# Performance work log

Measured on AMD Instinct MI355X. Metric: run time of the kernel, lower is better.

The kernel has to match this reference:

```python
import jax, jax.numpy as jnp
import numpy as np

B, T, F, H = 256, 512, 64, 128


def _uniform(key, shape, stdv):
    return jax.random.uniform(key, shape, jnp.float32, -stdv, stdv)


def setup_inputs() -> dict:
    key = jax.random.key(0)
    ks = jax.random.split(key, 24)
    values = jax.random.normal(ks[0], (B, T, F), jnp.float32)
    masks = (jax.random.uniform(ks[1], (B, T, F)) < 0.8).astype(jnp.float32)
    deltas = jax.random.uniform(ks[2], (B, T, F), jnp.float32)
    labels = (jax.random.uniform(ks[3], (B, 1)) < 0.5).astype(jnp.float32)
    is_train = (jax.random.uniform(ks[4], (B, 1)) < 0.8).astype(jnp.float32)
    sH = 1.0 / np.sqrt(H)
    sF = 1.0 / np.sqrt(F)
    # temp_decay_h: Linear F -> H (stdv = 1/sqrt(out) per reset_parameters)
    W_dh = _uniform(ks[5], (H, F), sH); b_dh = _uniform(ks[6], (H,), sH)
    # temp_decay_x: diag F -> F
    W_dx = _uniform(ks[7], (F, F), sF); b_dx = _uniform(ks[8], (F,), sF)
    # hist_reg: Linear H -> F (torch Linear stdv = 1/sqrt(in))
    W_hr = _uniform(ks[9], (F, H), sH); b_hr = _uniform(ks[10], (F,), sH)
    # feat_reg: F -> F with zeroed diagonal mask
    W_fr = _uniform(ks[11], (F, F), sF); b_fr = _uniform(ks[12], (F,), sF)
    # weight_combine: Linear 2F -> F
    s2F = 1.0 / np.sqrt(2 * F)
    W_wc = _uniform(ks[13], (F, 2 * F), s2F); b_wc = _uniform(ks[14], (F,), s2F)
    # LSTMCell(2F, H): torch init uniform(-1/sqrt(H), 1/sqrt(H)), gate order i,f,g,o
    W_ih = _uniform(ks[15], (4 * H, 2 * F), sH); b_ih = _uniform(ks[16], (4 * H,), sH)
    W_hh = _uniform(ks[17], (4 * H, H), sH); b_hh = _uniform(ks[18], (4 * H,), sH)
    # out: Linear H -> 1
    W_out = _uniform(ks[19], (1, H), sH); b_out = _uniform(ks[20], (1,), sH)
    return dict(values=values, masks=masks, deltas=deltas, labels=labels, is_train=is_train,
                W_dh=W_dh, b_dh=b_dh, W_dx=W_dx, b_dx=b_dx, W_hr=W_hr, b_hr=b_hr,
                W_fr=W_fr, b_fr=b_fr, W_wc=W_wc, b_wc=b_wc,
                W_ih=W_ih, b_ih=b_ih, W_hh=W_hh, b_hh=b_hh, W_out=W_out, b_out=b_out)


def _forward(values, masks, deltas, labels, is_train,
             W_dh, b_dh, W_dx, b_dx, W_hr, b_hr, W_fr, b_fr, W_wc, b_wc,
             W_ih, b_ih, W_hh, b_hh, W_out, b_out):
    eps = 1e-5
    w_dx_diag = jnp.diagonal(W_dx)            # diag mask: W * I
    W_fr_m = W_fr * (1.0 - jnp.eye(F, dtype=W_fr.dtype))  # zero diagonal

    def step(carry, xs):
        h, c, x_loss = carry
        x, m, d = xs                           # each [B, F]
        gamma_h = jnp.exp(-jax.nn.relu(d @ W_dh.T + b_dh))   # [B, H]
        gamma_x = jnp.exp(-jax.nn.relu(d * w_dx_diag + b_dx))  # [B, F]
        h = h * gamma_h
        x_h = h @ W_hr.T + b_hr                # [B, F]
        msum = jnp.sum(m) + eps
        x_loss = x_loss + jnp.sum(jnp.abs(x - x_h) * m) / msum
        x_c = m * x + (1.0 - m) * x_h
        z_h = x_c @ W_fr_m.T + b_fr
        x_loss = x_loss + jnp.sum(jnp.abs(x - z_h) * m) / msum
        alpha = jnp.concatenate([gamma_x, m], axis=1) @ W_wc.T + b_wc
        c_h = alpha * z_h + (1.0 - alpha) * x_h
        x_loss = x_loss + jnp.sum(jnp.abs(x - c_h) * m) / msum
        c_c = m * x + (1.0 - m) * c_h
        inp = jnp.concatenate([c_c, m], axis=1)   # [B, 2F]
        gates = inp @ W_ih.T + b_ih + h @ W_hh.T + b_hh  # [B, 4H]
        i, f, g, o = jnp.split(gates, 4, axis=1)
        c = jax.nn.sigmoid(f) * c + jax.nn.sigmoid(i) * jnp.tanh(g)
        h = jax.nn.sigmoid(o) * jnp.tanh(c)
        return (h, c, x_loss), c_c

    h0 = jnp.zeros((values.shape[0], H), values.dtype)
    c0 = jnp.zeros((values.shape[0], H), values.dtype)
    xs = (jnp.swapaxes(values, 0, 1), jnp.swapaxes(masks, 0, 1), jnp.swapaxes(deltas, 0, 1))
    (h, c, x_loss), imps = jax.lax.scan(step, (h0, c0, jnp.float32(0.0)), xs)
    imputations = jnp.swapaxes(imps, 0, 1)     # [B, T, F]
    y_h = h @ W_out.T + b_out                  # [B, 1] logits
    # stable BCE with logits (matches torch reference formula)
    max_val = jnp.maximum(-y_h, 0.0)
    y_l = y_h - y_h * labels + max_val + jnp.log(jnp.exp(-max_val) + jnp.exp(-y_h - max_val))
    y_loss = jnp.sum(y_l * is_train) / (jnp.sum(is_train) + eps)
    loss = x_loss / T + y_loss * 0.3
    predictions = jax.nn.sigmoid(y_h)
    return loss, predictions, imputations


def reference(values, masks, deltas, labels, is_train,
              W_dh, b_dh, W_dx, b_dx, W_hr, b_hr, W_fr, b_fr, W_wc, b_wc,
              W_ih, b_ih, W_hh, b_hh, W_out, b_out):
    return _forward(values, masks, deltas, labels, is_train,
                    W_dh, b_dh, W_dx, b_dx, W_hr, b_hr, W_fr, b_fr, W_wc, b_wc,
                    W_ih, b_ih, W_hh, b_hh, W_out, b_out)
```

## Files before the change

### kernel.cpp

```cpp
#include <hip/hip_runtime.h>
#include <hip/hip_fp16.h>


#define NBATCH 256
#define NT 512
#define NF 64
#define NH 128

#define WHH_OFF   0u
#define WIH_OFF   131072u
#define WHR_OFF   262144u
#define WFR_OFF   278528u
#define INVMS_OFF 286720u
#define ISTR_OFF  288768u
#define GH_OFF    294912u
#define AL_OFF    33849344u

typedef _Float16 half2_t __attribute__((ext_vector_type(2)));

__device__ __forceinline__ unsigned pack2(float a, float b) {
    __half2 h = __floats2half2_rn(a, b);
    return __builtin_bit_cast(unsigned, h);
}

__device__ __forceinline__ float dot2f(unsigned w, unsigned a, float acc) {
#if __has_builtin(__builtin_amdgcn_fdot2)
    return __builtin_amdgcn_fdot2(__builtin_bit_cast(half2_t, w),
                                  __builtin_bit_cast(half2_t, a), acc, false);
#else
    float2 wf = __half22float2(__builtin_bit_cast(__half2, w));
    float2 af = __half22float2(__builtin_bit_cast(__half2, a));
    return acc + wf.x * af.x + wf.y * af.y;
#endif
}

__device__ __forceinline__ float sigm(float x) { return 1.f / (1.f + __expf(-x)); }
__device__ __forceinline__ float tanh_fast(float x) { return 1.f - 2.f / (__expf(2.f * x) + 1.f); }

__global__ __launch_bounds__(256) void prep_w(const float* __restrict__ Whh,
                                              const float* __restrict__ Wih,
                                              const float* __restrict__ Whr,
                                              const float* __restrict__ Wfr,
                                              unsigned* __restrict__ wsu) {
    int o = blockIdx.x * 256 + threadIdx.x;
    float v0, v1;
    if (o < 32768) {
        int c = o & 3, r = (o >> 2) & 511, cb = o >> 11;
        int col = 8 * cb + 2 * c;
        v0 = Whh[r * 128 + col]; v1 = Whh[r * 128 + col + 1];
    } else if (o < 65536) {
        int o2 = o - 32768;
        int c = o2 & 3, r = (o2 >> 2) & 511, cb = o2 >> 11;
        int col = 8 * cb + 2 * c;
        v0 = Wih[r * 128 + col]; v1 = Wih[r * 128 + col + 1];
    } else if (o < 69632) {
        int o3 = o - 65536;
        int c = o3 & 3, f = (o3 >> 2) & 63, cb = o3 >> 8;
        int col = 8 * cb + 2 * c;
        v0 = Whr[f * 128 + col]; v1 = Whr[f * 128 + col + 1];
    } else if (o < 71680) {
        int o4 = o - 69632;
        int c = o4 & 3, f = (o4 >> 2) & 63, cb = o4 >> 8;
        int col = 8 * cb + 2 * c;
        v0 = (col == f) ? 0.f : Wfr[f * 64 + col];
        v1 = (col + 1 == f) ? 0.f : Wfr[f * 64 + col + 1];
    } else {
        return;
    }
    wsu[o] = pack2(v0, v1);
}

__global__ __launch_bounds__(256) void prep_msum(const float* __restrict__ masks,
                                                 const float* __restrict__ is_train,
                                                 float* __restrict__ invms,
                                                 float* __restrict__ inv_istr,
                                                 float* __restrict__ d_out0) {
    __shared__ float red[256];
    int tid = threadIdx.x;
    int t = blockIdx.x;
    if (t < NT) {
        int f = tid & 63, br = tid >> 6;
        float s = 0.f;
        for (int i = 0; i < 64; i++) {
            int b = br + i * 4;
            s += masks[((size_t)b * NT + t) * NF + f];
        }
        red[tid] = s;
        __syncthreads();
        for (int off = 128; off > 0; off >>= 1) {
            if (tid < off) red[tid] += red[tid + off];
            __syncthreads();
        }
        if (tid == 0) invms[t] = 1.f / (red[0] + 1e-5f);
    } else {
        red[tid] = is_train[tid];
        __syncthreads();
        for (int off = 128; off > 0; off >>= 1) {
            if (tid < off) red[tid] += red[tid + off];
            __syncthreads();
        }
        if (tid == 0) {
            *inv_istr = 1.f / (red[0] + 1e-5f);
            *d_out0 = 0.f;
        }
    }
}

__global__ __launch_bounds__(256) void ga_kernel(const float* __restrict__ deltas,
                                                 const float* __restrict__ masks,
                                                 const float* __restrict__ Wdh,
                                                 const float* __restrict__ bdh,
                                                 const float* __restrict__ Wdx,
                                                 const float* __restrict__ bdx,
                                                 const float* __restrict__ Wwc,
                                                 const float* __restrict__ bwc,
                                                 __half* __restrict__ gh_all,
                                                 __half* __restrict__ al_all) {
    __shared__ unsigned wdhpk[32 * 128];
    __shared__ unsigned wwcpk[64 * 64];
    __shared__ float sbdh[128], sbdx[64], swdx[64], sbwc[64];
    __shared__ float dbuf[64];
    __shared__ __align__(16) unsigned dpk[32], gxpk[32], mpk2[32];
    int tid = threadIdx.x;

    for (int o = tid; o < 4096; o += 256) {
        int j = o & 127, k2 = o >> 7;
        wdhpk[o] = pack2(Wdh[j * 64 + 2 * k2], Wdh[j * 64 + 2 * k2 + 1]);
    }
    for (int o = tid; o < 4096; o += 256) {
        int f = o & 63, k2 = o >> 6;
        wwcpk[o] = pack2(Wwc[f * 128 + 2 * k2], Wwc[f * 128 + 2 * k2 + 1]);
    }
    if (tid < 128) sbdh[tid] = bdh[tid];
    if (tid < 64) {
        sbdx[tid] = bdx[tid];
        swdx[tid] = Wdx[tid * 65];
        sbwc[tid] = bwc[tid];
    }
    __syncthreads();

    for (int i = 0; i < 32; i++) {
        int p = blockIdx.x * 32 + i;
        if (tid < 32) {
            float2 dv = ((const float2*)(deltas + (size_t)p * NF))[tid];
            dbuf[2 * tid] = dv.x; dbuf[2 * tid + 1] = dv.y;
            dpk[tid] = pack2(dv.x, dv.y);
        } else if (tid < 64) {
            int q = tid - 32;
            float2 mv = ((const float2*)(masks + (size_t)p * NF))[q];
            mpk2[q] = pack2(mv.x, mv.y);
        }
        __syncthreads();
        if (tid < 64) {
            float gx = __expf(-fmaxf(dbuf[tid] * swdx[tid] + sbdx[tid], 0.f));
            float oth = __shfl_xor(gx, 1);
            if (!(tid & 1)) gxpk[tid >> 1] = pack2(gx, oth);
        }
        __syncthreads();
        if (tid < 128) {
            float a0 = sbdh[tid], a1 = 0.f;
            #pragma unroll
            for (int k8 = 0; k8 < 8; k8++) {
                uint4 dp = *(const uint4*)&dpk[4 * k8];
                a0 = dot2f(wdhpk[(4 * k8 + 0) * 128 + tid], dp.x, a0);
                a1 = dot2f(wdhpk[(4 * k8 + 1) * 128 + tid], dp.y, a1);
                a0 = dot2f(wdhpk[(4 * k8 + 2) * 128 + tid], dp.z, a0);
                a1 = dot2f(wdhpk[(4 * k8 + 3) * 128 + tid], dp.w, a1);
            }
            gh_all[(size_t)p * NH + tid] = __float2half(__expf(-fmaxf(a0 + a1, 0.f)));
        } else if (tid < 192) {
            int f = tid - 128;
            float a0 = sbwc[f], a1 = 0.f;
            #pragma unroll
            for (int k8 = 0; k8 < 8; k8++) {
                uint4 gp = *(const uint4*)&gxpk[4 * k8];
                a0 = dot2f(wwcpk[(4 * k8 + 0) * 64 + f], gp.x, a0);
                a1 = dot2f(wwcpk[(4 * k8 + 1) * 64 + f], gp.y, a1);
                a0 = dot2f(wwcpk[(4 * k8 + 2) * 64 + f], gp.z, a0);
                a1 = dot2f(wwcpk[(4 * k8 + 3) * 64 + f], gp.w, a1);
            }
            #pragma unroll
            for (int k8 = 0; k8 < 8; k8++) {
                uint4 mp = *(const uint4*)&mpk2[4 * k8];
                a0 = dot2f(wwcpk[(32 + 4 * k8 + 0) * 64 + f], mp.x, a0);
                a1 = dot2f(wwcpk[(32 + 4 * k8 + 1) * 64 + f], mp.y, a1);
                a0 = dot2f(wwcpk[(32 + 4 * k8 + 2) * 64 + f], mp.z, a0);
                a1 = dot2f(wwcpk[(32 + 4 * k8 + 3) * 64 + f], mp.w, a1);
            }
            al_all[(size_t)p * NF + f] = __float2half(a0 + a1);
        }
        __syncthreads();
    }
}

__global__ __launch_bounds__(512, 2) void main_kernel(
    const float* __restrict__ values, const float* __restrict__ masks,
    const float* __restrict__ labels, const float* __restrict__ is_train,
    const float* __restrict__ b_hr, const float* __restrict__ b_fr,
    const float* __restrict__ b_ih, const float* __restrict__ b_hh,
    const float* __restrict__ W_out, const float* __restrict__ b_out,
    const uint4* __restrict__ whh_ws, const uint4* __restrict__ wih_ws,
    const uint4* __restrict__ whr_ws, const uint4* __restrict__ wfr_ws,
    const float* __restrict__ invms, const float* __restrict__ inv_istr,
    const __half* __restrict__ gh_all, const __half* __restrict__ al_all,
    float* __restrict__ d_out) {
    __shared__ uint4 whr4[16 * 64];
    __shared__ uint4 wfr4[8 * 64];
    __shared__ float bgate[512];
    __shared__ float sbhr[64], sbfr[64];
    __shared__ float hbuf[128], cbuf[128];
    __shared__ float mbuf[64];
    __shared__ __align__(16) unsigned hpk[64];
    __shared__ __align__(16) unsigned mpk[32], xcpk[32], ccpk[32];
    __shared__ float gates[512];

    const int tid = threadIdx.x;
    const int b = blockIdx.x;

    uint4 whh_r[16], wih_r[16];
    #pragma unroll
    for (int cb = 0; cb < 16; cb++) {
        whh_r[cb] = whh_ws[cb * 512 + tid];
        wih_r[cb] = wih_ws[cb * 512 + tid];
    }
    for (int o = tid; o < 1024; o += 512) whr4[o] = whr_ws[o];
    if (tid < 512) wfr4[tid] = wfr_ws[tid];
    bgate[tid] = b_ih[tid] + b_hh[tid];
    if (tid < 64) { sbhr[tid] = b_hr[tid]; sbfr[tid] = b_fr[tid]; }
    if (tid < 128) { hbuf[tid] = 0.f; cbuf[tid] = 0.f; }
    if (tid < 64) hpk[tid] = 0u;

    const float* vp = values + (size_t)b * NT * NF;
    const float* mp = masks + (size_t)b * NT * NF;
    const __half* alp = al_all + (size_t)b * NT * NF;
    const unsigned* ghu = (const unsigned*)(gh_all + (size_t)b * NT * NH);
    float* imp = d_out + 257 + (size_t)b * NT * NF;

    float lloss = 0.f;
    float xreg = 0.f, mreg = 0.f, xh_reg = 0.f;

    float xn = 0.f, aln = 0.f, invtn = 0.f;
    float2 mn = make_float2(0.f, 0.f);
    unsigned ghn = 0u;
    float alc = 0.f, invtc = 0.f;

    if (tid < 64) {
        xn = vp[tid];
        aln = __half2float(alp[tid]);
        invtn = invms[0];
    } else if (tid < 96) {
        mn = ((const float2*)mp)[tid - 64];
    } else if (tid < 160) {
        ghn = ghu[tid - 96];
    }
    __syncthreads();

    for (int t = 0; t < NT; t++) {
        if (tid < 64) {
            xreg = xn; alc = aln; invtc = invtn;
        } else if (tid < 96) {
            int q = tid - 64;
            mbuf[2 * q] = mn.x; mbuf[2 * q + 1] = mn.y;
            mpk[q] = pack2(mn.x, mn.y);
        } else if (tid < 160) {
            int q = tid - 96;
            float2 g = __half22float2(__builtin_bit_cast(__half2, ghn));
            float h0 = hbuf[2 * q] * g.x;
            float h1 = hbuf[2 * q + 1] * g.y;
            hbuf[2 * q] = h0; hbuf[2 * q + 1] = h1;
            hpk[q] = pack2(h0, h1);
        }
        __syncthreads();

        if (tid < 64) {
            int f = tid;
            mreg = mbuf[f];
            float a0 = sbhr[f], a1 = 0.f;
            #pragma unroll
            for (int k4 = 0; k4 < 16; k4 += 2) {
                uint4 w = whr4[k4 * 64 + f];
                uint4 hp = *(const uint4*)&hpk[4 * k4];
                a0 = dot2f(w.x, hp.x, a0); a0 = dot2f(w.y, hp.y, a0);
                a0 = dot2f(w.z, hp.z, a0); a0 = dot2f(w.w, hp.w, a0);
                uint4 w2 = whr4[(k4 + 1) * 64 + f];
                uint4 hp2 = *(const uint4*)&hpk[4 * k4 + 4];
                a1 = dot2f(w2.x, hp2.x, a1); a1 = dot2f(w2.y, hp2.y, a1);
                a1 = dot2f(w2.z, hp2.z, a1); a1 = dot2f(w2.w, hp2.w, a1);
            }
            xh_reg = a0 + a1;
            float xc = mreg * xreg + (1.f - mreg) * xh_reg;
            float oth = __shfl_xor(xc, 1);
            if (!(f & 1)) xcpk[f >> 1] = pack2(xc, oth);
        }
        __syncthreads();

        if (tid < 64) {
            int f = tid;
            float a0 = sbfr[f], a1 = 0.f;
            #pragma unroll
            for (int k4 = 0; k4 < 8; k4++) {
                uint4 w = wfr4[k4 * 64 + f];
                uint4 xp = *(const uint4*)&xcpk[4 * k4];
                a0 = dot2f(w.x, xp.x, a0); a1 = dot2f(w.y, xp.y, a1);
                a0 = dot2f(w.z, xp.z, a0); a1 = dot2f(w.w, xp.w, a1);
            }
            float zh = a0 + a1;
            float ch = alc * zh + (1.f - alc) * xh_reg;
            float cc = mreg * xreg + (1.f - mreg) * ch;
            imp[t * NF + f] = cc;
            lloss += (fabsf(xreg - xh_reg) + fabsf(xreg - zh) + fabsf(xreg - ch)) * mreg * invtc;
            float oth = __shfl_xor(cc, 1);
            if (!(f & 1)) ccpk[f >> 1] = pack2(cc, oth);
        }
        __syncthreads();

        {
            int tn = (t + 1 < NT) ? (t + 1) : (NT - 1);
            if (tid < 64) {
                xn = vp[tn * NF + tid];
                aln = __half2float(alp[tn * NF + tid]);
                invtn = invms[tn];
            } else if (tid < 96) {
                mn = ((const float2*)(mp + tn * NF))[tid - 64];
            } else if (tid < 160) {
                ghn = ghu[(size_t)tn * 64 + (tid - 96)];
            }

            float a0 = bgate[tid], a1 = 0.f, a2 = 0.f, a3 = 0.f;
            #pragma unroll
            for (int cb = 0; cb < 8; cb++) {
                uint4 ap = *(const uint4*)&ccpk[4 * cb];
                uint4 w = wih_r[cb];
                a0 = dot2f(w.x, ap.x, a0); a1 = dot2f(w.y, ap.y, a1);
                a2 = dot2f(w.z, ap.z, a2); a3 = dot2f(w.w, ap.w, a3);
            }
            #pragma unroll
            for (int cb = 0; cb < 8; cb++) {
                uint4 ap = *(const uint4*)&mpk[4 * cb];
                uint4 w = wih_r[8 + cb];
                a0 = dot2f(w.x, ap.x, a0); a1 = dot2f(w.y, ap.y, a1);
                a2 = dot2f(w.z, ap.z, a2); a3 = dot2f(w.w, ap.w, a3);
            }
            #pragma unroll
            for (int k4 = 0; k4 < 16; k4++) {
                uint4 hp = *(const uint4*)&hpk[4 * k4];
                uint4 w = whh_r[k4];
                a0 = dot2f(w.x, hp.x, a0); a1 = dot2f(w.y, hp.y, a1);
                a2 = dot2f(w.z, hp.z, a2); a3 = dot2f(w.w, hp.w, a3);
            }
            gates[tid] = (a0 + a1) + (a2 + a3);
        }
        __syncthreads();

        if (tid < 128) {
            float gi = gates[tid], gf = gates[128 + tid];
            float gg = gates[256 + tid], go = gates[384 + tid];
            float cn = sigm(gf) * cbuf[tid] + sigm(gi) * tanh_fast(gg);
            cbuf[tid] = cn;
            hbuf[tid] = sigm(go) * tanh_fast(cn);
        }
        __syncthreads();
    }

    if (tid < 64) {
        float ll = lloss;
        float yp = hbuf[tid] * W_out[tid] + hbuf[64 + tid] * W_out[64 + tid];
        #pragma unroll
        for (int off = 32; off > 0; off >>= 1) {
            ll += __shfl_down(ll, off);
            yp += __shfl_down(yp, off);
        }
        if (tid == 0) {
            float yh = yp + b_out[0];
            d_out[1 + b] = 1.f / (1.f + expf(-yh));
            float lab = labels[b], istr = is_train[b];
            float maxv = fmaxf(-yh, 0.f);
            float yl = yh - yh * lab + maxv + logf(expf(-maxv) + expf(-yh - maxv));
            atomicAdd(d_out, ll * (1.f / (float)NT) + 0.3f * yl * istr * (*inv_istr));
        }
    }
}

extern "C" void kernel_launch(void* const* d_in, const int* in_sizes, int n_in,
                              void* d_out, int out_size, void* d_ws, size_t ws_size,
                              hipStream_t stream) {
    const float* values = (const float*)d_in[0];
    const float* masks = (const float*)d_in[1];
    const float* deltas = (const float*)d_in[2];
    const float* labels = (const float*)d_in[3];
    const float* is_train = (const float*)d_in[4];
    const float* W_dh = (const float*)d_in[5];
    const float* b_dh = (const float*)d_in[6];
    const float* W_dx = (const float*)d_in[7];
    const float* b_dx = (const float*)d_in[8];
    const float* W_hr = (const float*)d_in[9];
    const float* b_hr = (const float*)d_in[10];
    const float* W_fr = (const float*)d_in[11];
    const float* b_fr = (const float*)d_in[12];
    const float* W_wc = (const float*)d_in[13];
    const float* b_wc = (const float*)d_in[14];
    const float* W_ih = (const float*)d_in[15];
    const float* b_ih = (const float*)d_in[16];
    const float* W_hh = (const float*)d_in[17];
    const float* b_hh = (const float*)d_in[18];
    const float* W_out = (const float*)d_in[19];
    const float* b_out = (const float*)d_in[20];

    char* ws = (char*)d_ws;
    unsigned* wsu = (unsigned*)d_ws;
    const uint4* whh_ws = (const uint4*)(ws + WHH_OFF);
    const uint4* wih_ws = (const uint4*)(ws + WIH_OFF);
    const uint4* whr_ws = (const uint4*)(ws + WHR_OFF);
    const uint4* wfr_ws = (const uint4*)(ws + WFR_OFF);
    float* invms = (float*)(ws + INVMS_OFF);
    float* inv_istr = (float*)(ws + ISTR_OFF);
    __half* gh_all = (__half*)(ws + GH_OFF);
    __half* al_all = (__half*)(ws + AL_OFF);
    float* out_f = (float*)d_out;

    prep_w<<<280, 256, 0, stream>>>(W_hh, W_ih, W_hr, W_fr, wsu);
    prep_msum<<<513, 256, 0, stream>>>(masks, is_train, invms, inv_istr, out_f);
    ga_kernel<<<4096, 256, 0, stream>>>(deltas, masks, W_dh, b_dh, W_dx, b_dx,
                                        W_wc, b_wc, gh_all, al_all);
    main_kernel<<<NBATCH, 512, 0, stream>>>(values, masks, labels, is_train,
                                            b_hr, b_fr, b_ih, b_hh, W_out, b_out,
                                            whh_ws, wih_ws, whr_ws, wfr_ws,
                                            invms, inv_istr, gh_all, al_all, out_f);
}
```

Baseline: 1.378 ms.

## Restructure LSTM step: split gate rows across 4 lanes, overlap Whh/Wih work, fewer barriers

Each hidden unit's four gate rows are now split across 4 threads, which keep the weight slices in registers and reduce partial sums with xor-shuffles. The LSTM cell update is fused into that same pass, so the gates shared buffer and one barrier go away. The Whh matvec and the hist_reg matvec, now spread across all 512 threads with a shared reduction, run before the serial feature-regression chain, and the mask term of Wih is computed by the idle warps while warp 0 does the regression. The decay gating of h is applied at the h-write point, and gh is prefetched several steps ahead. The intent is to shorten the serial per-step critical path, at the cost of more complex indexing and extra shuffles.

```diff
diff --git a/kernel.cpp b/kernel.cpp
--- a/kernel.cpp
+++ b/kernel.cpp
@@ -204,31 +204,43 @@
     const float* __restrict__ invms, const float* __restrict__ inv_istr,
     const __half* __restrict__ gh_all, const __half* __restrict__ al_all,
     float* __restrict__ d_out) {
-    __shared__ uint4 whr4[16 * 64];
     __shared__ uint4 wfr4[8 * 64];
-    __shared__ float bgate[512];
     __shared__ float sbhr[64], sbfr[64];
-    __shared__ float hbuf[128], cbuf[128];
-    __shared__ float mbuf[64];
     __shared__ __align__(16) unsigned hpk[64];
+    __shared__ float xp[512];
+    __shared__ float mbuf[64], xbuf[64], albuf[64];
     __shared__ __align__(16) unsigned mpk[32], xcpk[32], ccpk[32];
-    __shared__ float gates[512];
+    __shared__ __align__(16) unsigned ghpk[64];
+    __shared__ float hfin[128];
+    __shared__ float sinvt;
 
     const int tid = threadIdx.x;
     const int b = blockIdx.x;
-
-    uint4 whh_r[16], wih_r[16];
+    const int s = tid & 3;
+    const int cq = tid >> 2;
+    const int kg = tid >> 6;
+    const int fl = tid & 63;
+
+    uint4 whh_q[16];
+    uint4 wihc_q[8];
+    uint4 wihm_q[8];
+    float bg4[4];
     #pragma unroll
-    for (int cb = 0; cb < 16; cb++) {
-        whh_r[cb] = whh_ws[cb * 512 + tid];
-        wih_r[cb] = wih_ws[cb * 512 + tid];
-    }
-    for (int o = tid; o < 1024; o += 512) whr4[o] = whr_ws[o];
-    if (tid < 512) wfr4[tid] = wfr_ws[tid];
-    bgate[tid] = b_ih[tid] + b_hh[tid];
-    if (tid < 64) { sbhr[tid] = b_hr[tid]; sbfr[tid] = b_fr[tid]; }
-    if (tid < 128) { hbuf[tid] = 0.f; cbuf[tid] = 0.f; }
-    if (tid < 64) hpk[tid] = 0u;
+    for (int g = 0; g < 4; g++) {
+        int r = g * 128 + cq;
+        #pragma unroll
+        for (int j = 0; j < 4; j++) whh_q[g * 4 + j] = whh_ws[(4 * s + j) * 512 + r];
+        #pragma unroll
+        for (int j = 0; j < 2; j++) {
+            wihc_q[g * 2 + j] = wih_ws[(2 * s + j) * 512 + r];
+            wihm_q[g * 2 + j] = wih_ws[(8 + 2 * s + j) * 512 + r];
+        }
+        bg4[g] = b_ih[r] + b_hh[r];
+    }
+    uint4 whr_pa = whr_ws[(2 * kg) * 64 + fl];
+    uint4 whr_pb = whr_ws[(2 * kg + 1) * 64 + fl];
+    wfr4[tid] = wfr_ws[tid];
+    if (tid < 64) { sbhr[tid] = b_hr[tid]; sbfr[tid] = b_fr[tid]; hpk[tid] = 0u; }
 
     const float* vp = values + (size_t)b * NT * NF;
     const float* mp = masks + (size_t)b * NT * NF;
@@ -236,135 +248,164 @@
     const unsigned* ghu = (const unsigned*)(gh_all + (size_t)b * NT * NH);
     float* imp = d_out + 257 + (size_t)b * NT * NF;
 
+    float creg = 0.f;
     float lloss = 0.f;
-    float xreg = 0.f, mreg = 0.f, xh_reg = 0.f;
+    float hacc4[4] = {0.f, 0.f, 0.f, 0.f};
+    float macc4[4] = {0.f, 0.f, 0.f, 0.f};
 
     float xn = 0.f, aln = 0.f, invtn = 0.f;
     float2 mn = make_float2(0.f, 0.f);
-    unsigned ghn = 0u;
-    float alc = 0.f, invtc = 0.f;
-
-    if (tid < 64) {
-        xn = vp[tid];
-        aln = __half2float(alp[tid]);
-        invtn = invms[0];
-    } else if (tid < 96) {
-        mn = ((const float2*)mp)[tid - 64];
-    } else if (tid < 160) {
-        ghn = ghu[tid - 96];
+    unsigned ghA = 0u, ghB = 0u;
+    if (tid >= 256 && tid < 320) {
+        int q = tid - 256;
+        xn = vp[q];
+        aln = __half2float(alp[q]);
+        if (q == 0) invtn = invms[0];
+    } else if (tid >= 320 && tid < 352) {
+        mn = ((const float2*)mp)[tid - 320];
+    } else if (tid >= 352 && tid < 416) {
+        int q = tid - 352;
+        ghA = ghu[64 + q];
+        ghB = ghu[128 + q];
     }
     __syncthreads();
 
     for (int t = 0; t < NT; t++) {
-        if (tid < 64) {
-            xreg = xn; alc = aln; invtc = invtn;
-        } else if (tid < 96) {
-            int q = tid - 64;
+        if (tid >= 256 && tid < 320) {
+            int q = tid - 256;
+            xbuf[q] = xn; albuf[q] = aln;
+            if (q == 0) sinvt = invtn;
+        } else if (tid >= 320 && tid < 352) {
+            int q = tid - 320;
             mbuf[2 * q] = mn.x; mbuf[2 * q + 1] = mn.y;
             mpk[q] = pack2(mn.x, mn.y);
-        } else if (tid < 160) {
-            int q = tid - 96;
-            float2 g = __half22float2(__builtin_bit_cast(__half2, ghn));
-            float h0 = hbuf[2 * q] * g.x;
-            float h1 = hbuf[2 * q + 1] * g.y;
-            hbuf[2 * q] = h0; hbuf[2 * q + 1] = h1;
-            hpk[q] = pack2(h0, h1);
-        }
-        __syncthreads();
-
-        if (tid < 64) {
-            int f = tid;
-            mreg = mbuf[f];
-            float a0 = sbhr[f], a1 = 0.f;
-            #pragma unroll
-            for (int k4 = 0; k4 < 16; k4 += 2) {
-                uint4 w = whr4[k4 * 64 + f];
-                uint4 hp = *(const uint4*)&hpk[4 * k4];
-                a0 = dot2f(w.x, hp.x, a0); a0 = dot2f(w.y, hp.y, a0);
-                a0 = dot2f(w.z, hp.z, a0); a0 = dot2f(w.w, hp.w, a0);
-                uint4 w2 = whr4[(k4 + 1) * 64 + f];
-                uint4 hp2 = *(const uint4*)&hpk[4 * k4 + 4];
-                a1 = dot2f(w2.x, hp2.x, a1); a1 = dot2f(w2.y, hp2.y, a1);
-                a1 = dot2f(w2.z, hp2.z, a1); a1 = dot2f(w2.w, hp2.w, a1);
-            }
-            xh_reg = a0 + a1;
-            float xc = mreg * xreg + (1.f - mreg) * xh_reg;
-            float oth = __shfl_xor(xc, 1);
-            if (!(f & 1)) xcpk[f >> 1] = pack2(xc, oth);
-        }
-        __syncthreads();
-
-        if (tid < 64) {
-            int f = tid;
-            float a0 = sbfr[f], a1 = 0.f;
-            #pragma unroll
-            for (int k4 = 0; k4 < 8; k4++) {
-                uint4 w = wfr4[k4 * 64 + f];
-                uint4 xp = *(const uint4*)&xcpk[4 * k4];
-                a0 = dot2f(w.x, xp.x, a0); a1 = dot2f(w.y, xp.y, a1);
-                a0 = dot2f(w.z, xp.z, a0); a1 = dot2f(w.w, xp.w, a1);
-            }
-            float zh = a0 + a1;
-            float ch = alc * zh + (1.f - alc) * xh_reg;
-            float cc = mreg * xreg + (1.f - mreg) * ch;
-            imp[t * NF + f] = cc;
-            lloss += (fabsf(xreg - xh_reg) + fabsf(xreg - zh) + fabsf(xreg - ch)) * mreg * invtc;
-            float oth = __shfl_xor(cc, 1);
-            if (!(f & 1)) ccpk[f >> 1] = pack2(cc, oth);
-        }
-        __syncthreads();
-
+        }
         {
             int tn = (t + 1 < NT) ? (t + 1) : (NT - 1);
+            if (tid >= 256 && tid < 320) {
+                int q = tid - 256;
+                xn = vp[tn * NF + q];
+                aln = __half2float(alp[tn * NF + q]);
+                if (q == 0) invtn = invms[tn];
+            } else if (tid >= 320 && tid < 352) {
+                mn = ((const float2*)(mp + tn * NF))[tid - 320];
+            }
+        }
+        #pragma unroll
+        for (int g = 0; g < 4; g++) {
+            float u0 = 0.f, u1 = 0.f;
+            #pragma unroll
+            for (int j = 0; j < 4; j++) {
+                uint4 hq = *(const uint4*)&hpk[16 * s + 4 * j];
+                uint4 w = whh_q[g * 4 + j];
+                u0 = dot2f(w.x, hq.x, u0); u1 = dot2f(w.y, hq.y, u1);
+                u0 = dot2f(w.z, hq.z, u0); u1 = dot2f(w.w, hq.w, u1);
+            }
+            hacc4[g] = u0 + u1;
+        }
+        {
+            uint4 hpa = *(const uint4*)&hpk[8 * kg];
+            uint4 hpb = *(const uint4*)&hpk[8 * kg + 4];
+            float p0, p1;
+            p0 = dot2f(whr_pa.x, hpa.x, 0.f); p1 = dot2f(whr_pa.y, hpa.y, 0.f);
+            p0 = dot2f(whr_pa.z, hpa.z, p0);  p1 = dot2f(whr_pa.w, hpa.w, p1);
+            p0 = dot2f(whr_pb.x, hpb.x, p0);  p1 = dot2f(whr_pb.y, hpb.y, p1);
+            p0 = dot2f(whr_pb.z, hpb.z, p0);  p1 = dot2f(whr_pb.w, hpb.w, p1);
+            xp[tid] = p0 + p1;
+        }
+        __syncthreads();
+
+        if (tid < 64) {
+            __builtin_amdgcn_s_setprio(1);
+            float xh = sbhr[fl];
+            #pragma unroll
+            for (int g8 = 0; g8 < 8; g8++) xh += xp[g8 * 64 + fl];
+            float xv = xbuf[fl], mv = mbuf[fl], av = albuf[fl], it = sinvt;
+            float xc = mv * xv + (1.f - mv) * xh;
+            float oth = __shfl_xor(xc, 1);
+            if (!(fl & 1)) xcpk[fl >> 1] = pack2(xc, oth);
+            float b0 = sbfr[fl], b1 = 0.f;
+            #pragma unroll
+            for (int k4 = 0; k4 < 8; k4++) {
+                uint4 w = wfr4[k4 * 64 + fl];
+                uint4 xq = *(const uint4*)&xcpk[4 * k4];
+                b0 = dot2f(w.x, xq.x, b0); b1 = dot2f(w.y, xq.y, b1);
+                b0 = dot2f(w.z, xq.z, b0); b1 = dot2f(w.w, xq.w, b1);
+            }
+            float zh = b0 + b1;
+            float ch = av * zh + (1.f - av) * xh;
+            float cc = mv * xv + (1.f - mv) * ch;
+            imp[t * NF + fl] = cc;
+            lloss += (fabsf(xv - xh) + fabsf(xv - zh) + fabsf(xv - ch)) * mv * it;
+            oth = __shfl_xor(cc, 1);
+            if (!(fl & 1)) ccpk[fl >> 1] = pack2(cc, oth);
+            __builtin_amdgcn_s_setprio(0);
+        } else {
+            if (tid >= 352 && tid < 416) {
+                int q = tid - 352;
+                ghpk[q] = ghA;
+                ghA = ghB;
+                int tg = (t + 3 < NT) ? (t + 3) : (NT - 1);
+                ghB = ghu[(size_t)tg * 64 + q];
+            }
+            uint4 mq0 = *(const uint4*)&mpk[8 * s];
+            uint4 mq1 = *(const uint4*)&mpk[8 * s + 4];
+            #pragma unroll
+            for (int g = 0; g < 4; g++) {
+                uint4 wa = wihm_q[g * 2], wb = wihm_q[g * 2 + 1];
+                float u0 = dot2f(wa.x, mq0.x, 0.f), u1 = dot2f(wa.y, mq0.y, 0.f);
+                u0 = dot2f(wa.z, mq0.z, u0); u1 = dot2f(wa.w, mq0.w, u1);
+                u0 = dot2f(wb.x, mq1.x, u0); u1 = dot2f(wb.y, mq1.y, u1);
+                u0 = dot2f(wb.z, mq1.z, u0); u1 = dot2f(wb.w, mq1.w, u1);
+                macc4[g] = u0 + u1;
+            }
+        }
+        __syncthreads();
+
+        {
             if (tid < 64) {
-                xn = vp[tn * NF + tid];
-                aln = __half2float(alp[tn * NF + tid]);
-                invtn = invms[tn];
-            } else if (tid < 96) {
-                mn = ((const float2*)(mp + tn * NF))[tid - 64];
-            } else if (tid < 160) {
-                ghn = ghu[(size_t)tn * 64 + (tid - 96)];
-            }
-
-            float a0 = bgate[tid], a1 = 0.f, a2 = 0.f, a3 = 0.f;
-            #pragma unroll
-            for (int cb = 0; cb < 8; cb++) {
-                uint4 ap = *(const uint4*)&ccpk[4 * cb];
-                uint4 w = wih_r[cb];
-                a0 = dot2f(w.x, ap.x, a0); a1 = dot2f(w.y, ap.y, a1);
-                a2 = dot2f(w.z, ap.z, a2); a3 = dot2f(w.w, ap.w, a3);
-            }
-            #pragma unroll
-            for (int cb = 0; cb < 8; cb++) {
-                uint4 ap = *(const uint4*)&mpk[4 * cb];
-                uint4 w = wih_r[8 + cb];
-                a0 = dot2f(w.x, ap.x, a0); a1 = dot2f(w.y, ap.y, a1);
-                a2 = dot2f(w.z, ap.z, a2); a3 = dot2f(w.w, ap.w, a3);
-            }
-            #pragma unroll
-            for (int k4 = 0; k4 < 16; k4++) {
-                uint4 hp = *(const uint4*)&hpk[4 * k4];
-                uint4 w = whh_r[k4];
-                a0 = dot2f(w.x, hp.x, a0); a1 = dot2f(w.y, hp.y, a1);
-                a2 = dot2f(w.z, hp.z, a2); a3 = dot2f(w.w, hp.w, a3);
-            }
-            gates[tid] = (a0 + a1) + (a2 + a3);
-        }
-        __syncthreads();
-
-        if (tid < 128) {
-            float gi = gates[tid], gf = gates[128 + tid];
-            float gg = gates[256 + tid], go = gates[384 + tid];
-            float cn = sigm(gf) * cbuf[tid] + sigm(gi) * tanh_fast(gg);
-            cbuf[tid] = cn;
-            hbuf[tid] = sigm(go) * tanh_fast(cn);
+                uint4 mq0 = *(const uint4*)&mpk[8 * s];
+                uint4 mq1 = *(const uint4*)&mpk[8 * s + 4];
+                #pragma unroll
+                for (int g = 0; g < 4; g++) {
+                    uint4 wa = wihm_q[g * 2], wb = wihm_q[g * 2 + 1];
+                    float u0 = dot2f(wa.x, mq0.x, 0.f), u1 = dot2f(wa.y, mq0.y, 0.f);
+                    u0 = dot2f(wa.z, mq0.z, u0); u1 = dot2f(wa.w, mq0.w, u1);
+                    u0 = dot2f(wb.x, mq1.x, u0); u1 = dot2f(wb.y, mq1.y, u1);
+                    u0 = dot2f(wb.z, mq1.z, u0); u1 = dot2f(wb.w, mq1.w, u1);
+                    macc4[g] = u0 + u1;
+                }
+            }
+            uint4 cq0 = *(const uint4*)&ccpk[8 * s];
+            uint4 cq1 = *(const uint4*)&ccpk[8 * s + 4];
+            float gate[4];
+            #pragma unroll
+            for (int g = 0; g < 4; g++) {
+                uint4 wa = wihc_q[g * 2], wb = wihc_q[g * 2 + 1];
+                float u0 = dot2f(wa.x, cq0.x, 0.f), u1 = dot2f(wa.y, cq0.y, 0.f);
+                u0 = dot2f(wa.z, cq0.z, u0); u1 = dot2f(wa.w, cq0.w, u1);
+                u0 = dot2f(wb.x, cq1.x, u0); u1 = dot2f(wb.y, cq1.y, u1);
+                u0 = dot2f(wb.z, cq1.z, u0); u1 = dot2f(wb.w, cq1.w, u1);
+                float v = hacc4[g] + macc4[g] + (u0 + u1);
+                v += __shfl_xor(v, 1);
+                v += __shfl_xor(v, 2);
+                gate[g] = v + bg4[g];
+            }
+            float cn = sigm(gate[1]) * creg + sigm(gate[0]) * tanh_fast(gate[2]);
+            creg = cn;
+            float hn = sigm(gate[3]) * tanh_fast(cn);
+            float gm = __half2float(((const __half*)ghpk)[cq]);
+            float hd = hn * gm;
+            float oth = __shfl_xor(hd, 4);
+            if (!(tid & 7)) hpk[tid >> 3] = pack2(hd, oth);
+            if (t == NT - 1 && !(tid & 3)) hfin[cq] = hn;
         }
         __syncthreads();
     }
 
     if (tid < 64) {
         float ll = lloss;
-        float yp = hbuf[tid] * W_out[tid] + hbuf[64 + tid] * W_out[64 + tid];
+        float yp = hfin[tid] * W_out[tid] + hfin[64 + tid] * W_out[64 + tid];
         #pragma unroll
         for (int off = 32; off > 0; off >>= 1) {
             ll += __shfl_down(ll, off);
```

Measured after the change: 1.372 ms. No clear change (-0.5%).

## Batch 16 sequences per block and compute LSTM recurrence with MFMA

Applied to the files above, without the earlier changes.

The main recurrent kernel now processes 16 batch rows per workgroup instead of one. All per-step matvecs (hist_reg, feat_reg, W_ih, W_hh) become 16x16x32 f16 MFMA ops, with weights held in registers as B fragments. Inputs are staged four timesteps at a time through shared memory, the gamma decay is fused into the hidden-state write, and the loss reduction is restructured. The launch drops from 256 blocks to 16 on a chip with many CUs, so parallelism falls sharply in exchange for tensor-core throughput and fewer barriers per batch row.

```diff
diff --git a/kernel.cpp b/kernel.cpp
--- a/kernel.cpp
+++ b/kernel.cpp
@@ -6,6 +6,7 @@
 #define NT 512
 #define NF 64
 #define NH 128
+#define BPB 16
 
 #define WHH_OFF   0u
 #define WIH_OFF   131072u
@@ -16,6 +17,8 @@
 #define GH_OFF    294912u
 #define AL_OFF    33849344u
 
+typedef _Float16 f16x8 __attribute__((ext_vector_type(8)));
+typedef float f32x4 __attribute__((ext_vector_type(4)));
 typedef _Float16 half2_t __attribute__((ext_vector_type(2)));
 
 __device__ __forceinline__ unsigned pack2(float a, float b) {
@@ -24,18 +27,19 @@
 }
 
 __device__ __forceinline__ float dot2f(unsigned w, unsigned a, float acc) {
-#if __has_builtin(__builtin_amdgcn_fdot2)
-    return __builtin_amdgcn_fdot2(__builtin_bit_cast(half2_t, w),
-                                  __builtin_bit_cast(half2_t, a), acc, false);
-#else
     float2 wf = __half22float2(__builtin_bit_cast(__half2, w));
     float2 af = __half22float2(__builtin_bit_cast(__half2, a));
-    return acc + wf.x * af.x + wf.y * af.y;
-#endif
+    return fmaf(wf.x, af.x, fmaf(wf.y, af.y, acc));
 }
 
 __device__ __forceinline__ float sigm(float x) { return 1.f / (1.f + __expf(-x)); }
 __device__ __forceinline__ float tanh_fast(float x) { return 1.f - 2.f / (__expf(2.f * x) + 1.f); }
+
+__device__ __forceinline__ f16x8 as_h8(uint4 u) { return __builtin_bit_cast(f16x8, u); }
+
+__device__ __forceinline__ f16x8 ldA(const __half* row, int lg, int q) {
+    return as_h8(*(const uint4*)(row + q * 32 + lg * 8));
+}
 
 __global__ __launch_bounds__(256) void prep_w(const float* __restrict__ Whh,
                                               const float* __restrict__ Wih,
@@ -193,7 +197,7 @@
     }
 }
 
-__global__ __launch_bounds__(512, 2) void main_kernel(
+__global__ __launch_bounds__(512, 1) void main_kernel(
     const float* __restrict__ values, const float* __restrict__ masks,
     const float* __restrict__ labels, const float* __restrict__ is_train,
     const float* __restrict__ b_hr, const float* __restrict__ b_fr,
@@ -204,180 +208,226 @@
     const float* __restrict__ invms, const float* __restrict__ inv_istr,
     const __half* __restrict__ gh_all, const __half* __restrict__ al_all,
     float* __restrict__ d_out) {
-    __shared__ uint4 whr4[16 * 64];
-    __shared__ uint4 wfr4[8 * 64];
-    __shared__ float bgate[512];
-    __shared__ float sbhr[64], sbfr[64];
-    __shared__ float hbuf[128], cbuf[128];
-    __shared__ float mbuf[64];
-    __shared__ __align__(16) unsigned hpk[64];
-    __shared__ __align__(16) unsigned mpk[32], xcpk[32], ccpk[32];
-    __shared__ float gates[512];
+    __shared__ __align__(16) __half hdp[BPB][136];
+    __shared__ __align__(16) __half xcp[BPB][72];
+    __shared__ __align__(16) __half ccp[BPB][72];
+    __shared__ float xs[4][BPB][68], ms[4][BPB][68];
+    __shared__ __align__(16) __half als[4][BPB][72];
+    __shared__ __align__(16) __half mp16[4][BPB][72];
+    __shared__ __align__(16) __half gams[4][BPB][136];
+    __shared__ float sinv4[4];
+    __shared__ float hfin[BPB][128];
+    __shared__ float redl[512];
+    __shared__ float ylarr[BPB];
 
     const int tid = threadIdx.x;
-    const int b = blockIdx.x;
-
-    uint4 whh_r[16], wih_r[16];
+    const int w = tid >> 6;
+    const int l = tid & 63;
+    const int lr = l & 15;
+    const int lg = l >> 4;
+    const int b0 = blockIdx.x * BPB;
+    const int fcol = w * 16 + lr;
+
+    uint4 whhB[4][4];
+    uint4 wicB[4][2];
+    uint4 wimB[4][2];
+    float bg4[4];
     #pragma unroll
-    for (int cb = 0; cb < 16; cb++) {
-        whh_r[cb] = whh_ws[cb * 512 + tid];
-        wih_r[cb] = wih_ws[cb * 512 + tid];
-    }
-    for (int o = tid; o < 1024; o += 512) whr4[o] = whr_ws[o];
-    if (tid < 512) wfr4[tid] = wfr_ws[tid];
-    bgate[tid] = b_ih[tid] + b_hh[tid];
-    if (tid < 64) { sbhr[tid] = b_hr[tid]; sbfr[tid] = b_fr[tid]; }
-    if (tid < 128) { hbuf[tid] = 0.f; cbuf[tid] = 0.f; }
-    if (tid < 64) hpk[tid] = 0u;
-
-    const float* vp = values + (size_t)b * NT * NF;
-    const float* mp = masks + (size_t)b * NT * NF;
-    const __half* alp = al_all + (size_t)b * NT * NF;
-    const unsigned* ghu = (const unsigned*)(gh_all + (size_t)b * NT * NH);
-    float* imp = d_out + 257 + (size_t)b * NT * NF;
-
+    for (int g = 0; g < 4; g++) {
+        int n = g * 128 + w * 16 + lr;
+        #pragma unroll
+        for (int q = 0; q < 4; q++) whhB[g][q] = whh_ws[(q * 4 + lg) * 512 + n];
+        #pragma unroll
+        for (int q = 0; q < 2; q++) {
+            wicB[g][q] = wih_ws[(q * 4 + lg) * 512 + n];
+            wimB[g][q] = wih_ws[((q + 2) * 4 + lg) * 512 + n];
+        }
+        bg4[g] = b_ih[n] + b_hh[n];
+    }
+    uint4 whrB[4], wfrB[2];
+    float bhr_r = 0.f, bfr_r = 0.f;
+    if (w < 4) {
+        #pragma unroll
+        for (int q = 0; q < 4; q++) whrB[q] = whr_ws[(q * 4 + lg) * 64 + fcol];
+        #pragma unroll
+        for (int q = 0; q < 2; q++) wfrB[q] = wfr_ws[(q * 4 + lg) * 64 + fcol];
+        bhr_r = b_hr[fcol];
+        bfr_r = b_fr[fcol];
+    }
+
+    for (int i = tid; i < BPB * 136; i += 512) ((__half*)hdp)[i] = __float2half(0.f);
+
+    const int bq = tid >> 5;
+    const int fq = (tid & 31) * 2;
+    const int cq4 = (tid & 31) * 4;
+    const float* vpb = values + (size_t)(b0 + bq) * NT * NF;
+    const float* mpb = masks + (size_t)(b0 + bq) * NT * NF;
+    const __half* apb = al_all + (size_t)(b0 + bq) * NT * NF;
+    const __half* gpb = gh_all + (size_t)(b0 + bq) * NT * NH;
+    float* impb = d_out + 257;
+
+    float2 xr4[4], mr4[4];
+    unsigned ar4[4];
+    uint2 gr4[4];
+    float ir4[4] = {0.f, 0.f, 0.f, 0.f};
+    #pragma unroll
+    for (int u = 0; u < 4; u++) {
+        xr4[u] = *(const float2*)(vpb + (size_t)u * NF + fq);
+        mr4[u] = *(const float2*)(mpb + (size_t)u * NF + fq);
+        ar4[u] = *(const unsigned*)(apb + (size_t)u * NF + fq);
+        gr4[u] = *(const uint2*)(gpb + (size_t)(u + 1) * NH + cq4);
+    }
+    if (tid == 0) {
+        #pragma unroll
+        for (int u = 0; u < 4; u++) ir4[u] = invms[u];
+    }
+
+    float c4[4] = {0.f, 0.f, 0.f, 0.f};
     float lloss = 0.f;
-    float xreg = 0.f, mreg = 0.f, xh_reg = 0.f;
-
-    float xn = 0.f, aln = 0.f, invtn = 0.f;
-    float2 mn = make_float2(0.f, 0.f);
-    unsigned ghn = 0u;
-    float alc = 0.f, invtc = 0.f;
-
-    if (tid < 64) {
-        xn = vp[tid];
-        aln = __half2float(alp[tid]);
-        invtn = invms[0];
-    } else if (tid < 96) {
-        mn = ((const float2*)mp)[tid - 64];
-    } else if (tid < 160) {
-        ghn = ghu[tid - 96];
-    }
     __syncthreads();
 
-    for (int t = 0; t < NT; t++) {
-        if (tid < 64) {
-            xreg = xn; alc = aln; invtc = invtn;
-        } else if (tid < 96) {
-            int q = tid - 64;
-            mbuf[2 * q] = mn.x; mbuf[2 * q + 1] = mn.y;
-            mpk[q] = pack2(mn.x, mn.y);
-        } else if (tid < 160) {
-            int q = tid - 96;
-            float2 g = __half22float2(__builtin_bit_cast(__half2, ghn));
-            float h0 = hbuf[2 * q] * g.x;
-            float h1 = hbuf[2 * q + 1] * g.y;
-            hbuf[2 * q] = h0; hbuf[2 * q + 1] = h1;
-            hpk[q] = pack2(h0, h1);
-        }
-        __syncthreads();
-
-        if (tid < 64) {
-            int f = tid;
-            mreg = mbuf[f];
-            float a0 = sbhr[f], a1 = 0.f;
-            #pragma unroll
-            for (int k4 = 0; k4 < 16; k4 += 2) {
-                uint4 w = whr4[k4 * 64 + f];
-                uint4 hp = *(const uint4*)&hpk[4 * k4];
-                a0 = dot2f(w.x, hp.x, a0); a0 = dot2f(w.y, hp.y, a0);
-                a0 = dot2f(w.z, hp.z, a0); a0 = dot2f(w.w, hp.w, a0);
-                uint4 w2 = whr4[(k4 + 1) * 64 + f];
-                uint4 hp2 = *(const uint4*)&hpk[4 * k4 + 4];
-                a1 = dot2f(w2.x, hp2.x, a1); a1 = dot2f(w2.y, hp2.y, a1);
-                a1 = dot2f(w2.z, hp2.z, a1); a1 = dot2f(w2.w, hp2.w, a1);
-            }
-            xh_reg = a0 + a1;
-            float xc = mreg * xreg + (1.f - mreg) * xh_reg;
-            float oth = __shfl_xor(xc, 1);
-            if (!(f & 1)) xcpk[f >> 1] = pack2(xc, oth);
-        }
-        __syncthreads();
-
-        if (tid < 64) {
-            int f = tid;
-            float a0 = sbfr[f], a1 = 0.f;
-            #pragma unroll
-            for (int k4 = 0; k4 < 8; k4++) {
-                uint4 w = wfr4[k4 * 64 + f];
-                uint4 xp = *(const uint4*)&xcpk[4 * k4];
-                a0 = dot2f(w.x, xp.x, a0); a1 = dot2f(w.y, xp.y, a1);
-                a0 = dot2f(w.z, xp.z, a0); a1 = dot2f(w.w, xp.w, a1);
-            }
-            float zh = a0 + a1;
-            float ch = alc * zh + (1.f - alc) * xh_reg;
-            float cc = mreg * xreg + (1.f - mreg) * ch;
-            imp[t * NF + f] = cc;
-            lloss += (fabsf(xreg - xh_reg) + fabsf(xreg - zh) + fabsf(xreg - ch)) * mreg * invtc;
-            float oth = __shfl_xor(cc, 1);
-            if (!(f & 1)) ccpk[f >> 1] = pack2(cc, oth);
-        }
-        __syncthreads();
-
-        {
-            int tn = (t + 1 < NT) ? (t + 1) : (NT - 1);
-            if (tid < 64) {
-                xn = vp[tn * NF + tid];
-                aln = __half2float(alp[tn * NF + tid]);
-                invtn = invms[tn];
-            } else if (tid < 96) {
-                mn = ((const float2*)(mp + tn * NF))[tid - 64];
-            } else if (tid < 160) {
-                ghn = ghu[(size_t)tn * 64 + (tid - 96)];
-            }
-
-            float a0 = bgate[tid], a1 = 0.f, a2 = 0.f, a3 = 0.f;
-            #pragma unroll
-            for (int cb = 0; cb < 8; cb++) {
-                uint4 ap = *(const uint4*)&ccpk[4 * cb];
-                uint4 w = wih_r[cb];
-                a0 = dot2f(w.x, ap.x, a0); a1 = dot2f(w.y, ap.y, a1);
-                a2 = dot2f(w.z, ap.z, a2); a3 = dot2f(w.w, ap.w, a3);
-            }
-            #pragma unroll
-            for (int cb = 0; cb < 8; cb++) {
-                uint4 ap = *(const uint4*)&mpk[4 * cb];
-                uint4 w = wih_r[8 + cb];
-                a0 = dot2f(w.x, ap.x, a0); a1 = dot2f(w.y, ap.y, a1);
-                a2 = dot2f(w.z, ap.z, a2); a3 = dot2f(w.w, ap.w, a3);
-            }
-            #pragma unroll
-            for (int k4 = 0; k4 < 16; k4++) {
-                uint4 hp = *(const uint4*)&hpk[4 * k4];
-                uint4 w = whh_r[k4];
-                a0 = dot2f(w.x, hp.x, a0); a1 = dot2f(w.y, hp.y, a1);
-                a2 = dot2f(w.z, hp.z, a2); a3 = dot2f(w.w, hp.w, a3);
-            }
-            gates[tid] = (a0 + a1) + (a2 + a3);
-        }
-        __syncthreads();
-
-        if (tid < 128) {
-            float gi = gates[tid], gf = gates[128 + tid];
-            float gg = gates[256 + tid], go = gates[384 + tid];
-            float cn = sigm(gf) * cbuf[tid] + sigm(gi) * tanh_fast(gg);
-            cbuf[tid] = cn;
-            hbuf[tid] = sigm(go) * tanh_fast(cn);
-        }
-        __syncthreads();
-    }
-
-    if (tid < 64) {
-        float ll = lloss;
-        float yp = hbuf[tid] * W_out[tid] + hbuf[64 + tid] * W_out[64 + tid];
-        #pragma unroll
-        for (int off = 32; off > 0; off >>= 1) {
-            ll += __shfl_down(ll, off);
-            yp += __shfl_down(yp, off);
-        }
-        if (tid == 0) {
-            float yh = yp + b_out[0];
-            d_out[1 + b] = 1.f / (1.f + expf(-yh));
-            float lab = labels[b], istr = is_train[b];
-            float maxv = fmaxf(-yh, 0.f);
-            float yl = yh - yh * lab + maxv + logf(expf(-maxv) + expf(-yh - maxv));
-            atomicAdd(d_out, ll * (1.f / (float)NT) + 0.3f * yl * istr * (*inv_istr));
-        }
+    for (int tb = 0; tb < NT; tb += 4) {
+        #pragma unroll
+        for (int j = 0; j < 4; j++) {
+            const int t = tb + j;
+            f32x4 accg[4] = {{0.f,0.f,0.f,0.f},{0.f,0.f,0.f,0.f},
+                             {0.f,0.f,0.f,0.f},{0.f,0.f,0.f,0.f}};
+            f32x4 accx = {0.f, 0.f, 0.f, 0.f};
+
+            if (j == 0) {
+                #pragma unroll
+                for (int u = 0; u < 4; u++) {
+                    xs[u][bq][fq] = xr4[u].x; xs[u][bq][fq + 1] = xr4[u].y;
+                    ms[u][bq][fq] = mr4[u].x; ms[u][bq][fq + 1] = mr4[u].y;
+                    *(unsigned*)&als[u][bq][fq] = ar4[u];
+                    *(unsigned*)&mp16[u][bq][fq] = pack2(mr4[u].x, mr4[u].y);
+                    *(uint2*)&gams[u][bq][cq4] = gr4[u];
+                }
+                if (tid == 0) {
+                    #pragma unroll
+                    for (int u = 0; u < 4; u++) sinv4[u] = ir4[u];
+                }
+                #pragma unroll
+                for (int u = 0; u < 4; u++) {
+                    int tn = tb + 4 + u; if (tn > NT - 1) tn = NT - 1;
+                    int tg = tb + 5 + u; if (tg > NT - 1) tg = NT - 1;
+                    xr4[u] = *(const float2*)(vpb + (size_t)tn * NF + fq);
+                    mr4[u] = *(const float2*)(mpb + (size_t)tn * NF + fq);
+                    ar4[u] = *(const unsigned*)(apb + (size_t)tn * NF + fq);
+                    gr4[u] = *(const uint2*)(gpb + (size_t)tg * NH + cq4);
+                }
+                if (tid == 0) {
+                    #pragma unroll
+                    for (int u = 0; u < 4; u++) {
+                        int tn = tb + 4 + u; if (tn > NT - 1) tn = NT - 1;
+                        ir4[u] = invms[tn];
+                    }
+                }
+            }
+            #pragma unroll
+            for (int q = 0; q < 4; q++) {
+                f16x8 a = ldA(&hdp[lr][0], lg, q);
+                #pragma unroll
+                for (int g = 0; g < 4; g++)
+                    accg[g] = __builtin_amdgcn_mfma_f32_16x16x32_f16(a, as_h8(whhB[g][q]), accg[g], 0, 0, 0);
+                if (w < 4)
+                    accx = __builtin_amdgcn_mfma_f32_16x16x32_f16(a, as_h8(whrB[q]), accx, 0, 0, 0);
+            }
+            __syncthreads();
+
+            float xh4[4], xv4[4], mv4[4];
+            if (w < 4) {
+                #pragma unroll
+                for (int e = 0; e < 4; e++) {
+                    int r = lg * 4 + e;
+                    float xv = xs[j][r][fcol], mv = ms[j][r][fcol];
+                    float xh = accx[e] + bhr_r;
+                    float xc = mv * xv + (1.f - mv) * xh;
+                    xcp[r][fcol] = __float2half(xc);
+                    xh4[e] = xh; xv4[e] = xv; mv4[e] = mv;
+                }
+            }
+            #pragma unroll
+            for (int q = 0; q < 2; q++) {
+                f16x8 a = ldA(&mp16[j][lr][0], lg, q);
+                #pragma unroll
+                for (int g = 0; g < 4; g++)
+                    accg[g] = __builtin_amdgcn_mfma_f32_16x16x32_f16(a, as_h8(wimB[g][q]), accg[g], 0, 0, 0);
+            }
+            __syncthreads();
+
+            if (w < 4) {
+                f32x4 accz = {0.f, 0.f, 0.f, 0.f};
+                #pragma unroll
+                for (int q = 0; q < 2; q++) {
+                    f16x8 a = ldA(&xcp[lr][0], lg, q);
+                    accz = __builtin_amdgcn_mfma_f32_16x16x32_f16(a, as_h8(wfrB[q]), accz, 0, 0, 0);
+                }
+                float sv = sinv4[j];
+                #pragma unroll
+                for (int e = 0; e < 4; e++) {
+                    int r = lg * 4 + e;
+                    float av = __half2float(als[j][r][fcol]);
+                    float zh = accz[e] + bfr_r;
+                    float ch = av * zh + (1.f - av) * xh4[e];
+                    float cc = mv4[e] * xv4[e] + (1.f - mv4[e]) * ch;
+                    lloss += (fabsf(xv4[e] - xh4[e]) + fabsf(xv4[e] - zh) +
+                              fabsf(xv4[e] - ch)) * mv4[e] * sv;
+                    impb[((size_t)(b0 + r) * NT + t) * NF + fcol] = cc;
+                    ccp[r][fcol] = __float2half(cc);
+                }
+            }
+            __syncthreads();
+
+            #pragma unroll
+            for (int q = 0; q < 2; q++) {
+                f16x8 a = ldA(&ccp[lr][0], lg, q);
+                #pragma unroll
+                for (int g = 0; g < 4; g++)
+                    accg[g] = __builtin_amdgcn_mfma_f32_16x16x32_f16(a, as_h8(wicB[g][q]), accg[g], 0, 0, 0);
+            }
+            {
+                const int cell = w * 16 + lr;
+                #pragma unroll
+                for (int e = 0; e < 4; e++) {
+                    int r = lg * 4 + e;
+                    float gi = accg[0][e] + bg4[0];
+                    float gf = accg[1][e] + bg4[1];
+                    float gg = accg[2][e] + bg4[2];
+                    float go = accg[3][e] + bg4[3];
+                    float cn = sigm(gf) * c4[e] + sigm(gi) * tanh_fast(gg);
+                    c4[e] = cn;
+                    float hn = sigm(go) * tanh_fast(cn);
+                    float gm = __half2float(gams[j][r][cell]);
+                    hdp[r][cell] = __float2half(hn * gm);
+                    if (t == NT - 1) hfin[r][cell] = hn;
+                }
+            }
+            __syncthreads();
+        }
+    }
+
+    redl[tid] = lloss;
+    __syncthreads();
+    for (int off = 256; off > 0; off >>= 1) {
+        if (tid < off) redl[tid] += redl[tid + off];
+        __syncthreads();
+    }
+    if (tid < BPB) {
+        float yp = 0.f;
+        for (int c = 0; c < 128; c++) yp += hfin[tid][c] * W_out[c];
+        float yh = yp + b_out[0];
+        d_out[1 + b0 + tid] = 1.f / (1.f + expf(-yh));
+        float lab = labels[b0 + tid], istr = is_train[b0 + tid];
+        float maxv = fmaxf(-yh, 0.f);
+        float yl = yh - yh * lab + maxv + logf(expf(-maxv) + expf(-yh - maxv));
+        ylarr[tid] = yl * istr;
+    }
+    __syncthreads();
+    if (tid == 0) {
+        float s = 0.f;
+        for (int i = 0; i < BPB; i++) s += ylarr[i];
+        atomicAdd(d_out, redl[0] * (1.f / (float)NT) + 0.3f * s * (*inv_istr));
     }
 }
 
@@ -422,8 +472,9 @@
     prep_msum<<<513, 256, 0, stream>>>(masks, is_train, invms, inv_istr, out_f);
     ga_kernel<<<4096, 256, 0, stream>>>(deltas, masks, W_dh, b_dh, W_dx, b_dx,
                                         W_wc, b_wc, gh_all, al_all);
-    main_kernel<<<NBATCH, 512, 0, stream>>>(values, masks, labels, is_train,
-                                            b_hr, b_fr, b_ih, b_hh, W_out, b_out,
-                                            whh_ws, wih_ws, whr_ws, wfr_ws,
-                                            invms, inv_istr, gh_all, al_all, out_f);
-}
+    main_kernel<<<NBATCH / BPB, 512, 0, stream>>>(values, masks, labels, is_train,
+                                                  b_hr, b_fr, b_ih, b_hh, W_out, b_out,
+                                                  whh_ws, wih_ws, whr_ws, wfr_ws,
+                                                  invms, inv_istr, gh_all, al_all,
+                                                  out_f);
+}
```

Result: slower. 2.116 ms (+53.6%).
